# Performance work log

Measured on AMD Instinct MI355X. Metric: run time of the kernel, lower is better.

Reference implementation:

```python
import jax, jax.numpy as jnp
import numpy as np
import math

N_HEADS = 8

def setup_inputs() -> dict:
    key = jax.random.key(0)
    qkv = jax.random.normal(key, (4, 1536, 2048), dtype=jnp.float32)
    return {"qkv": qkv}

def reference(qkv):
    bs, width, length = qkv.shape
    ch = width // (3 * N_HEADS)
    # reshape to [bs*n_heads, 3*ch, length] then split into q, k, v
    qkv_h = qkv.reshape(bs * N_HEADS, 3 * ch, length)
    q = qkv_h[:, :ch]
    k = qkv_h[:, ch:2 * ch]
    v = qkv_h[:, 2 * ch:]
    scale = 1.0 / math.sqrt(math.sqrt(ch))
    # scores: [B*H, T, S]
    weight = jnp.einsum('bct,bcs->bts', q * scale, k * scale)
    weight = jax.nn.softmax(weight.astype(jnp.float32), axis=-1).astype(weight.dtype)
    a = jnp.einsum('bts,bcs->bct', weight, v)  # [B*H, ch, T]
    return a.reshape(bs, N_HEADS * ch, length)
```

## Files before the change

kernel.cpp:

```cpp
#include <hip/hip_runtime.h>
#include <hip/hip_bf16.h>

typedef __attribute__((ext_vector_type(8))) short bf16x8;
typedef __attribute__((ext_vector_type(8))) unsigned short u16x8;
typedef __attribute__((ext_vector_type(4))) float f32x4;
typedef __attribute__((ext_vector_type(16))) float f32x16;

#define SEQ 2048
#define NBH 32
#define QSCALE 0.1803368801111204f

#if __has_builtin(__builtin_amdgcn_exp2f)
#define EXP2(x) __builtin_amdgcn_exp2f(x)
#else
#define EXP2(x) exp2f(x)
#endif

__device__ __forceinline__ unsigned short bfc(float f) {
  union { __hip_bfloat16 h; unsigned short u; } v;
  v.h = __float2bfloat16(f);
  return v.u;
}

__global__ __launch_bounds__(256)
void prep_kernel(const float* __restrict__ qkv, unsigned short* __restrict__ ws) {
  const int tid = threadIdx.x;
  const int b = blockIdx.x;
  if (b < 4096) {
    int gid = b * 256 + tid;
    int sec = gid >> 19;
    int r = gid & 524287;
    int bh = r >> 14;
    int rr = r & 16383;
    int cc = rr >> 11;
    int t = rr & 2047;
    const float* src = qkv + ((size_t)(bh >> 3) * 1536 + (bh & 7) * 192 + sec * 64 + cc * 8) * SEQ + t;
    const float scale = sec ? 1.0f : QSCALE;
    u16x8 o;
    #pragma unroll
    for (int e = 0; e < 8; ++e) o[e] = bfc(src[(size_t)e * SEQ] * scale);
    if (sec == 0) {
      unsigned short* dst = ws + ((size_t)bh * SEQ + t) * 64;
      *(u16x8*)(dst + ((cc ^ (t & 7)) * 8)) = o;
    } else {
      const int tile = t >> 6, shh = (t >> 5) & 1, lww = t & 31;
      const int kc = cc >> 1, hh = cc & 1;
      unsigned short* dst = ws + (size_t)NBH * SEQ * 64 + (size_t)bh * SEQ * 64;
      const int idx = ((tile * 2 + shh) * 4 + kc) * 64 + hh * 32 + lww;
      *(u16x8*)(dst + (size_t)idx * 8) = o;
    }
  } else {
    int cid = (b - 4096) * 256 + tid;
    int bh = cid >> 14;
    int rr = cid & 16383;
    int c = rr >> 8;
    int cc = rr & 255;
    int tile = cc >> 3, sub = cc & 7;
    const float* src = qkv + ((size_t)(bh >> 3) * 1536 + (bh & 7) * 192 + 128 + c) * SEQ + cc * 8;
    float4 a = *(const float4*)(src);
    float4 bv = *(const float4*)(src + 4);
    u16x8 o;
    o[0] = bfc(a.x); o[1] = bfc(a.y); o[2] = bfc(a.z); o[3] = bfc(a.w);
    o[4] = bfc(bv.x); o[5] = bfc(bv.y); o[6] = bfc(bv.z); o[7] = bfc(bv.w);
    const int shh = sub >> 2, ks = (sub >> 1) & 1, hh = sub & 1;
    const int ch = c >> 5, lww = c & 31;
    unsigned short* dst = ws + (size_t)2 * NBH * SEQ * 64 + (size_t)bh * SEQ * 64;
    const int idx = (((tile * 2 + shh) * 2 + ch) * 2 + ks) * 64 + hh * 32 + lww;
    *(u16x8*)(dst + (size_t)idx * 8) = o;
  }
}

__global__ __launch_bounds__(256, 2)
void attn_main(const unsigned short* __restrict__ ws, float* __restrict__ out) {
  const int bid = blockIdx.x;
  const int bh = (bid & 7) + 8 * ((bid >> 3) >> 4);
  const int tile0 = (bid >> 3) & 15;
  const int t0 = tile0 * 128;

  const unsigned short* Qws = ws + ((size_t)bh * SEQ + t0) * 64;
  const unsigned short* Kf = ws + (size_t)NBH * SEQ * 64 + (size_t)bh * SEQ * 64;
  const unsigned short* Vf = ws + (size_t)2 * NBH * SEQ * 64 + (size_t)bh * SEQ * 64;
  float* __restrict__ outb = out + (size_t)bh * 64 * SEQ;

  __shared__ __align__(16) float red[8192];

  const int tid = threadIdx.x;
  const int w = tid >> 6;
  const int ts = w & 1;
  const int sh = w >> 1;
  const int l = tid & 63;
  const int lw = l & 31;
  const int h = l >> 5;
  const int sw = lw & 7;

  bf16x8 qB[2][4];
  #pragma unroll
  for (int tsub = 0; tsub < 2; ++tsub) {
    const int rloc = ts * 64 + tsub * 32 + lw;
    #pragma unroll
    for (int kc = 0; kc < 4; ++kc)
      qB[tsub][kc] = *(const bf16x8*)&Qws[rloc * 64 + (((2 * kc + h) ^ sw) * 8)];
  }

  f32x16 zero16;
  #pragma unroll
  for (int i = 0; i < 16; ++i) zero16[i] = 0.f;
  bf16x8 onesB;
  #pragma unroll
  for (int i = 0; i < 8; ++i) onesB[i] = (short)0x3F80;

  f32x16 accO[2][2];
  f32x16 psum[2];
  accO[0][0] = zero16; accO[0][1] = zero16;
  accO[1][0] = zero16; accO[1][1] = zero16;
  psum[0] = zero16; psum[1] = zero16;

  bf16x8 ka[4];
  #pragma unroll
  for (int kc = 0; kc < 4; ++kc)
    ka[kc] = *(const bf16x8*)&Kf[(size_t)((sh * 4 + kc) * 64 + l) * 8];

  #pragma unroll 1
  for (int it = 0; it < SEQ / 64; ++it) {
    bf16x8 kan[4];
    {
      const int itn = (it + 1) & 31;
      #pragma unroll
      for (int kc = 0; kc < 4; ++kc)
        kan[kc] = *(const bf16x8*)&Kf[(size_t)(((itn * 2 + sh) * 4 + kc) * 64 + l) * 8];
    }
    bf16x8 vB[2][2];
    #pragma unroll
    for (int ch = 0; ch < 2; ++ch)
      #pragma unroll
      for (int ks = 0; ks < 2; ++ks)
        vB[ch][ks] = *(const bf16x8*)&Vf[(size_t)(((((it * 2 + sh) * 2 + ch) * 2 + ks)) * 64 + l) * 8];

    f32x16 accS[2];
    #pragma unroll
    for (int kc = 0; kc < 4; ++kc) {
      #pragma unroll
      for (int tsub = 0; tsub < 2; ++tsub)
        accS[tsub] = __builtin_amdgcn_mfma_f32_32x32x16_bf16(
            ka[kc], qB[tsub][kc], kc ? accS[tsub] : zero16, 0, 0, 0);
    }

    #pragma unroll
    for (int tsub = 0; tsub < 2; ++tsub)
      #pragma unroll
      for (int r = 0; r < 16; ++r) accS[tsub][r] = EXP2(accS[tsub][r]);

    bf16x8 pA[2][2];
    #pragma unroll
    for (int tsub = 0; tsub < 2; ++tsub) {
      unsigned int pk[8];
      #pragma unroll
      for (int wd = 0; wd < 8; ++wd)
        asm("v_cvt_pk_bf16_f32 %0, %1, %2"
            : "=v"(pk[wd]) : "v"(accS[tsub][2 * wd]), "v"(accS[tsub][2 * wd + 1]));
      #pragma unroll
      for (int a = 0; a < 2; ++a) {
        unsigned int x0 = pk[4 * a + 0], y0 = pk[4 * a + 2];
        unsigned int x1 = pk[4 * a + 1], y1 = pk[4 * a + 3];
        asm("v_permlane32_swap_b32 %0, %1" : "+v"(x0), "+v"(y0));
        asm("v_permlane32_swap_b32 %0, %1" : "+v"(x1), "+v"(y1));
        union { unsigned int u[4]; bf16x8 v; } uu;
        uu.u[0] = x0; uu.u[1] = x1; uu.u[2] = y0; uu.u[3] = y1;
        pA[tsub][a] = uu.v;
      }
    }

    #pragma unroll
    for (int tsub = 0; tsub < 2; ++tsub)
      #pragma unroll
      for (int ks = 0; ks < 2; ++ks)
        psum[tsub] = __builtin_amdgcn_mfma_f32_32x32x16_bf16(pA[tsub][ks], onesB, psum[tsub], 0, 0, 0);

    #pragma unroll
    for (int ch = 0; ch < 2; ++ch) {
      #pragma unroll
      for (int ks = 0; ks < 2; ++ks) {
        #pragma unroll
        for (int tsub = 0; tsub < 2; ++tsub)
          accO[tsub][ch] = __builtin_amdgcn_mfma_f32_32x32x16_bf16(pA[tsub][ks], vB[ch][ks], accO[tsub][ch], 0, 0, 0);
      }
    }

    ka[0] = kan[0]; ka[1] = kan[1]; ka[2] = kan[2]; ka[3] = kan[3];
  }

  if (sh == 1) {
    #pragma unroll
    for (int tsub = 0; tsub < 2; ++tsub)
      #pragma unroll
      for (int ch = 0; ch < 2; ++ch)
        #pragma unroll
        for (int r = 0; r < 16; ++r)
          red[(((ts * 2 + tsub) * 2 + ch) * 16 + r) * 64 + l] = accO[tsub][ch][r];
  }
  __syncthreads();
  if (sh == 0) {
    #pragma unroll
    for (int tsub = 0; tsub < 2; ++tsub)
      #pragma unroll
      for (int ch = 0; ch < 2; ++ch)
        #pragma unroll
        for (int r = 0; r < 16; ++r)
          accO[tsub][ch][r] += red[(((ts * 2 + tsub) * 2 + ch) * 16 + r) * 64 + l];
  }
  __syncthreads();
  if (sh == 1) {
    #pragma unroll
    for (int tsub = 0; tsub < 2; ++tsub)
      #pragma unroll
      for (int r = 0; r < 16; ++r)
        red[((ts * 2 + tsub) * 16 + r) * 64 + l] = psum[tsub][r];
  }
  __syncthreads();
  if (sh == 0) {
    #pragma unroll
    for (int tsub = 0; tsub < 2; ++tsub) {
      float linv[16];
      #pragma unroll
      for (int r = 0; r < 16; ++r)
        linv[r] = 1.0f / (psum[tsub][r] + red[((ts * 2 + tsub) * 16 + r) * 64 + l]);
      #pragma unroll
      for (int ch = 0; ch < 2; ++ch) {
        #pragma unroll
        for (int r = 0; r < 16; ++r) {
          const int tg = t0 + ts * 64 + tsub * 32 + (r & 3) + 8 * (r >> 2) + 4 * h;
          outb[(size_t)(32 * ch + lw) * SEQ + tg] = accO[tsub][ch][r] * linv[r];
        }
      }
    }
  }
}

#define PAD 72
#define BTF 128
__device__ __forceinline__ unsigned short f2bf(float f) {
  union { float f; unsigned u; } v; v.f = f;
  return (unsigned short)((v.u + 0x7fffu + ((v.u >> 16) & 1u)) >> 16);
}

__global__ __launch_bounds__(512, 4)
void qkv_attn_fallback(const float* __restrict__ qkv, float* __restrict__ out) {
  const int bid = blockIdx.x;
  const int xcd = bid & 7;
  const int slot = bid >> 3;
  const int bh = xcd + 8 * (slot >> 4);
  const int tile = slot & 15;
  const int t0 = tile * BTF;

  const float* __restrict__ base = qkv + (size_t)((bh >> 3) * 1536 + (bh & 7) * 192) * SEQ;
  const float* __restrict__ qg = base;
  const float* __restrict__ kg = base + 64 * SEQ;
  const float* __restrict__ vg = base + 128 * SEQ;
  float* __restrict__ outb = out + (size_t)bh * 64 * SEQ;

  __shared__ __align__(16) unsigned short Qt[BTF * PAD];
  __shared__ __align__(16) unsigned short Kt[64 * PAD];
  __shared__ __align__(16) unsigned short Vt[64 * PAD];
  __shared__ __align__(16) unsigned short Pl[BTF * PAD];

  const int tid = threadIdx.x;
  const int w = tid >> 6;
  const int l = tid & 63;
  const int lr = l & 15;
  const int g = l >> 4;

  {
    const int cb = tid >> 5, tb = tid & 31;
    const int c0 = cb * 4, tt0 = tb * 4;
    const float* p = qg + c0 * SEQ + t0 + tt0;
    float4 r0 = *(const float4*)(p);
    float4 r1 = *(const float4*)(p + SEQ);
    float4 r2 = *(const float4*)(p + 2 * SEQ);
    float4 r3 = *(const float4*)(p + 3 * SEQ);
    const float s = 0.125f;
    ushort4 w0 = { f2bf(r0.x*s), f2bf(r1.x*s), f2bf(r2.x*s), f2bf(r3.x*s) };
    ushort4 w1 = { f2bf(r0.y*s), f2bf(r1.y*s), f2bf(r2.y*s), f2bf(r3.y*s) };
    ushort4 w2 = { f2bf(r0.z*s), f2bf(r1.z*s), f2bf(r2.z*s), f2bf(r3.z*s) };
    ushort4 w3 = { f2bf(r0.w*s), f2bf(r1.w*s), f2bf(r2.w*s), f2bf(r3.w*s) };
    *(ushort4*)&Qt[(tt0 + 0) * PAD + c0] = w0;
    *(ushort4*)&Qt[(tt0 + 1) * PAD + c0] = w1;
    *(ushort4*)&Qt[(tt0 + 2) * PAD + c0] = w2;
    *(ushort4*)&Qt[(tt0 + 3) * PAD + c0] = w3;
  }
  __syncthreads();

  bf16x8 qB0 = *(const bf16x8*)&Qt[(w * 16 + lr) * PAD + g * 8];
  bf16x8 qB1 = *(const bf16x8*)&Qt[(w * 16 + lr) * PAD + g * 8 + 32];

  f32x4 pv[4];
  #pragma unroll
  for (int i = 0; i < 4; ++i) pv[i] = (f32x4){0.f, 0.f, 0.f, 0.f};
  float mrun = -1e30f;
  float lsum = 0.f;

  for (int s0 = 0; s0 < SEQ; s0 += 64) {
    __syncthreads();
    {
      const int cb = tid >> 4, sb = tid & 15;
      const int c0 = cb * 2, sl = sb * 4;
      const float* p0 = kg + c0 * SEQ + s0 + sl;
      float4 a0 = *(const float4*)(p0);
      float4 a1 = *(const float4*)(p0 + SEQ);
      ushort2 y0 = { f2bf(a0.x), f2bf(a1.x) };
      ushort2 y1 = { f2bf(a0.y), f2bf(a1.y) };
      ushort2 y2 = { f2bf(a0.z), f2bf(a1.z) };
      ushort2 y3 = { f2bf(a0.w), f2bf(a1.w) };
      *(ushort2*)&Kt[(sl + 0) * PAD + c0] = y0;
      *(ushort2*)&Kt[(sl + 1) * PAD + c0] = y1;
      *(ushort2*)&Kt[(sl + 2) * PAD + c0] = y2;
      *(ushort2*)&Kt[(sl + 3) * PAD + c0] = y3;
    }
    {
      const int c = tid >> 3;
      const int sq = (tid & 7) * 8;
      const float* p0 = vg + c * SEQ + s0 + sq;
      float4 b0 = *(const float4*)(p0);
      float4 b1 = *(const float4*)(p0 + 4);
      ushort4 z0 = { f2bf(b0.x), f2bf(b0.y), f2bf(b0.z), f2bf(b0.w) };
      ushort4 z1 = { f2bf(b1.x), f2bf(b1.y), f2bf(b1.z), f2bf(b1.w) };
      *(ushort4*)&Vt[c * PAD + sq] = z0;
      *(ushort4*)&Vt[c * PAD + sq + 4] = z1;
    }
    __syncthreads();

    f32x4 acc[4];
    #pragma unroll
    for (int i = 0; i < 4; ++i) acc[i] = (f32x4){0.f, 0.f, 0.f, 0.f};
    #pragma unroll
    for (int ch = 0; ch < 2; ++ch) {
      bf16x8 qb = ch ? qB1 : qB0;
      #pragma unroll
      for (int sub = 0; sub < 4; ++sub) {
        bf16x8 ka = *(const bf16x8*)&Kt[(sub * 16 + lr) * PAD + g * 8 + 32 * ch];
        acc[sub] = __builtin_amdgcn_mfma_f32_16x16x32_bf16(ka, qb, acc[sub], 0, 0, 0);
      }
    }

    float pmax = -1e30f;
    #pragma unroll
    for (int sub = 0; sub < 4; ++sub)
      #pragma unroll
      for (int r = 0; r < 4; ++r) pmax = fmaxf(pmax, acc[sub][r]);
    pmax = fmaxf(pmax, __shfl_xor(pmax, 16));
    pmax = fmaxf(pmax, __shfl_xor(pmax, 32));
    const float mnew = fmaxf(mrun, pmax);
    const float alpha = __expf(mrun - mnew);
    float rsum = 0.f;
    #pragma unroll
    for (int sub = 0; sub < 4; ++sub) {
      #pragma unroll
      for (int r = 0; r < 4; ++r) {
        float p = __expf(acc[sub][r] - mnew);
        acc[sub][r] = p;
        rsum += p;
      }
    }
    rsum += __shfl_xor(rsum, 16);
    rsum += __shfl_xor(rsum, 32);
    lsum = lsum * alpha + rsum;
    mrun = mnew;

    #pragma unroll
    for (int sub = 0; sub < 4; ++sub) {
      ushort4 pw = { f2bf(acc[sub][0]), f2bf(acc[sub][1]), f2bf(acc[sub][2]), f2bf(acc[sub][3]) };
      *(ushort4*)&Pl[(w * 16 + lr) * PAD + sub * 16 + g * 4] = pw;
    }

    {
      const int sbase = (l & 48) + g * 4;
      #pragma unroll
      for (int r = 0; r < 4; ++r) {
        float ar = __shfl(alpha, sbase + r, 64);
        #pragma unroll
        for (int cs = 0; cs < 4; ++cs) pv[cs][r] *= ar;
      }
    }

    bf16x8 pA0 = *(const bf16x8*)&Pl[(w * 16 + lr) * PAD + g * 8];
    bf16x8 pA1 = *(const bf16x8*)&Pl[(w * 16 + lr) * PAD + g * 8 + 32];
    #pragma unroll
    for (int cs = 0; cs < 4; ++cs) {
      bf16x8 v0 = *(const bf16x8*)&Vt[(cs * 16 + lr) * PAD + g * 8];
      bf16x8 v1 = *(const bf16x8*)&Vt[(cs * 16 + lr) * PAD + g * 8 + 32];
      pv[cs] = __builtin_amdgcn_mfma_f32_16x16x32_bf16(pA0, v0, pv[cs], 0, 0, 0);
      pv[cs] = __builtin_amdgcn_mfma_f32_16x16x32_bf16(pA1, v1, pv[cs], 0, 0, 0);
    }
  }

  {
    const int sbase = (l & 48) + g * 4;
    float linv[4];
    #pragma unroll
    for (int r = 0; r < 4; ++r) linv[r] = 1.0f / __shfl(lsum, sbase + r, 64);
    #pragma unroll
    for (int cs = 0; cs < 4; ++cs) {
      #pragma unroll
      for (int r = 0; r < 4; ++r) {
        outb[(cs * 16 + lr) * SEQ + t0 + w * 16 + g * 4 + r] = pv[cs][r] * linv[r];
      }
    }
  }
}

extern "C" void kernel_launch(void* const* d_in, const int* in_sizes, int n_in,
                              void* d_out, int out_size, void* d_ws, size_t ws_size,
                              hipStream_t stream) {
  const float* qkv = (const float*)d_in[0];
  float* out = (float*)d_out;
  const size_t need = (size_t)3 * NBH * SEQ * 64 * sizeof(unsigned short);
  if (ws_size >= need) {
    unsigned short* ws = (unsigned short*)d_ws;
    prep_kernel<<<dim3(6144), dim3(256), 0, stream>>>(qkv, ws);
    attn_main<<<dim3(512), dim3(256), 0, stream>>>(ws, out);
  } else {
    qkv_attn_fallback<<<dim3(512), dim3(512), 0, stream>>>(qkv, out);
  }
}
```

Before: 65.01 us.

## Halve query tile per block to double grid and raise occupancy

The attention kernel's query tile per block drops from 128 to 64 rows, so each wave handles one 32-row subtile instead of two. The grid doubles to 1024 blocks, the shared reduction buffer halves, and launch bounds now allow 4 blocks per CU, aiming for more resident waves and better latency hiding. In exchange, each K/V tile is loaded twice as often per query row, which raises global/L2 traffic, and MFMA reuse of each K/V fragment is halved.

New measurement: 70.96 us. +9.2%, slower.

```diff
diff --git a/kernel.cpp b/kernel.cpp
--- a/kernel.cpp
+++ b/kernel.cpp
@@ -70,19 +70,19 @@
   }
 }
 
-__global__ __launch_bounds__(256, 2)
+__global__ __launch_bounds__(256, 4)
 void attn_main(const unsigned short* __restrict__ ws, float* __restrict__ out) {
   const int bid = blockIdx.x;
-  const int bh = (bid & 7) + 8 * ((bid >> 3) >> 4);
-  const int tile0 = (bid >> 3) & 15;
-  const int t0 = tile0 * 128;
+  const int bh = (bid & 7) + 8 * ((bid >> 3) >> 5);
+  const int tile0 = (bid >> 3) & 31;
+  const int t0 = tile0 * 64;
 
   const unsigned short* Qws = ws + ((size_t)bh * SEQ + t0) * 64;
   const unsigned short* Kf = ws + (size_t)NBH * SEQ * 64 + (size_t)bh * SEQ * 64;
   const unsigned short* Vf = ws + (size_t)2 * NBH * SEQ * 64 + (size_t)bh * SEQ * 64;
   float* __restrict__ outb = out + (size_t)bh * 64 * SEQ;
 
-  __shared__ __align__(16) float red[8192];
+  __shared__ __align__(16) float red[4096];
 
   const int tid = threadIdx.x;
   const int w = tid >> 6;
@@ -93,13 +93,12 @@
   const int h = l >> 5;
   const int sw = lw & 7;
 
-  bf16x8 qB[2][4];
-  #pragma unroll
-  for (int tsub = 0; tsub < 2; ++tsub) {
-    const int rloc = ts * 64 + tsub * 32 + lw;
+  bf16x8 qB[4];
+  {
+    const int rloc = ts * 32 + lw;
     #pragma unroll
     for (int kc = 0; kc < 4; ++kc)
-      qB[tsub][kc] = *(const bf16x8*)&Qws[rloc * 64 + (((2 * kc + h) ^ sw) * 8)];
+      qB[kc] = *(const bf16x8*)&Qws[rloc * 64 + (((2 * kc + h) ^ sw) * 8)];
   }
 
   f32x16 zero16;
@@ -109,11 +108,9 @@
   #pragma unroll
   for (int i = 0; i < 8; ++i) onesB[i] = (short)0x3F80;
 
-  f32x16 accO[2][2];
-  f32x16 psum[2];
-  accO[0][0] = zero16; accO[0][1] = zero16;
-  accO[1][0] = zero16; accO[1][1] = zero16;
-  psum[0] = zero16; psum[1] = zero16;
+  f32x16 accO[2];
+  f32x16 psum;
+  accO[0] = zero16; accO[1] = zero16; psum = zero16;
 
   bf16x8 ka[4];
   #pragma unroll
@@ -136,28 +133,21 @@
       for (int ks = 0; ks < 2; ++ks)
         vB[ch][ks] = *(const bf16x8*)&Vf[(size_t)(((((it * 2 + sh) * 2 + ch) * 2 + ks)) * 64 + l) * 8];
 
-    f32x16 accS[2];
-    #pragma unroll
-    for (int kc = 0; kc < 4; ++kc) {
-      #pragma unroll
-      for (int tsub = 0; tsub < 2; ++tsub)
-        accS[tsub] = __builtin_amdgcn_mfma_f32_32x32x16_bf16(
-            ka[kc], qB[tsub][kc], kc ? accS[tsub] : zero16, 0, 0, 0);
-    }
-
-    #pragma unroll
-    for (int tsub = 0; tsub < 2; ++tsub)
-      #pragma unroll
-      for (int r = 0; r < 16; ++r) accS[tsub][r] = EXP2(accS[tsub][r]);
-
-    bf16x8 pA[2][2];
-    #pragma unroll
-    for (int tsub = 0; tsub < 2; ++tsub) {
+    f32x16 accS;
+    #pragma unroll
+    for (int kc = 0; kc < 4; ++kc)
+      accS = __builtin_amdgcn_mfma_f32_32x32x16_bf16(ka[kc], qB[kc], kc ? accS : zero16, 0, 0, 0);
+
+    #pragma unroll
+    for (int r = 0; r < 16; ++r) accS[r] = EXP2(accS[r]);
+
+    bf16x8 pA[2];
+    {
       unsigned int pk[8];
       #pragma unroll
       for (int wd = 0; wd < 8; ++wd)
         asm("v_cvt_pk_bf16_f32 %0, %1, %2"
-            : "=v"(pk[wd]) : "v"(accS[tsub][2 * wd]), "v"(accS[tsub][2 * wd + 1]));
+            : "=v"(pk[wd]) : "v"(accS[2 * wd]), "v"(accS[2 * wd + 1]));
       #pragma unroll
       for (int a = 0; a < 2; ++a) {
         unsigned int x0 = pk[4 * a + 0], y0 = pk[4 * a + 2];
@@ -166,71 +156,56 @@
         asm("v_permlane32_swap_b32 %0, %1" : "+v"(x1), "+v"(y1));
         union { unsigned int u[4]; bf16x8 v; } uu;
         uu.u[0] = x0; uu.u[1] = x1; uu.u[2] = y0; uu.u[3] = y1;
-        pA[tsub][a] = uu.v;
-      }
-    }
-
-    #pragma unroll
-    for (int tsub = 0; tsub < 2; ++tsub)
+        pA[a] = uu.v;
+      }
+    }
+
+    #pragma unroll
+    for (int ks = 0; ks < 2; ++ks)
+      psum = __builtin_amdgcn_mfma_f32_32x32x16_bf16(pA[ks], onesB, psum, 0, 0, 0);
+
+    #pragma unroll
+    for (int ch = 0; ch < 2; ++ch)
       #pragma unroll
       for (int ks = 0; ks < 2; ++ks)
-        psum[tsub] = __builtin_amdgcn_mfma_f32_32x32x16_bf16(pA[tsub][ks], onesB, psum[tsub], 0, 0, 0);
-
-    #pragma unroll
-    for (int ch = 0; ch < 2; ++ch) {
-      #pragma unroll
-      for (int ks = 0; ks < 2; ++ks) {
-        #pragma unroll
-        for (int tsub = 0; tsub < 2; ++tsub)
-          accO[tsub][ch] = __builtin_amdgcn_mfma_f32_32x32x16_bf16(pA[tsub][ks], vB[ch][ks], accO[tsub][ch], 0, 0, 0);
-      }
-    }
+        accO[ch] = __builtin_amdgcn_mfma_f32_32x32x16_bf16(pA[ks], vB[ch][ks], accO[ch], 0, 0, 0);
 
     ka[0] = kan[0]; ka[1] = kan[1]; ka[2] = kan[2]; ka[3] = kan[3];
   }
 
   if (sh == 1) {
     #pragma unroll
-    for (int tsub = 0; tsub < 2; ++tsub)
-      #pragma unroll
-      for (int ch = 0; ch < 2; ++ch)
-        #pragma unroll
-        for (int r = 0; r < 16; ++r)
-          red[(((ts * 2 + tsub) * 2 + ch) * 16 + r) * 64 + l] = accO[tsub][ch][r];
+    for (int ch = 0; ch < 2; ++ch)
+      #pragma unroll
+      for (int r = 0; r < 16; ++r)
+        red[((ts * 2 + ch) * 16 + r) * 64 + l] = accO[ch][r];
   }
   __syncthreads();
   if (sh == 0) {
     #pragma unroll
-    for (int tsub = 0; tsub < 2; ++tsub)
-      #pragma unroll
-      for (int ch = 0; ch < 2; ++ch)
-        #pragma unroll
-        for (int r = 0; r < 16; ++r)
-          accO[tsub][ch][r] += red[(((ts * 2 + tsub) * 2 + ch) * 16 + r) * 64 + l];
+    for (int ch = 0; ch < 2; ++ch)
+      #pragma unroll
+      for (int r = 0; r < 16; ++r)
+        accO[ch][r] += red[((ts * 2 + ch) * 16 + r) * 64 + l];
   }
   __syncthreads();
   if (sh == 1) {
     #pragma unroll
-    for (int tsub = 0; tsub < 2; ++tsub)
-      #pragma unroll
-      for (int r = 0; r < 16; ++r)
-        red[((ts * 2 + tsub) * 16 + r) * 64 + l] = psum[tsub][r];
+    for (int r = 0; r < 16; ++r)
+      red[(ts * 16 + r) * 64 + l] = psum[r];
   }
   __syncthreads();
   if (sh == 0) {
-    #pragma unroll
-    for (int tsub = 0; tsub < 2; ++tsub) {
-      float linv[16];
-      #pragma unroll
-      for (int r = 0; r < 16; ++r)
-        linv[r] = 1.0f / (psum[tsub][r] + red[((ts * 2 + tsub) * 16 + r) * 64 + l]);
-      #pragma unroll
-      for (int ch = 0; ch < 2; ++ch) {
-        #pragma unroll
-        for (int r = 0; r < 16; ++r) {
-          const int tg = t0 + ts * 64 + tsub * 32 + (r & 3) + 8 * (r >> 2) + 4 * h;
-          outb[(size_t)(32 * ch + lw) * SEQ + tg] = accO[tsub][ch][r] * linv[r];
-        }
+    float linv[16];
+    #pragma unroll
+    for (int r = 0; r < 16; ++r)
+      linv[r] = 1.0f / (psum[r] + red[(ts * 16 + r) * 64 + l]);
+    #pragma unroll
+    for (int ch = 0; ch < 2; ++ch) {
+      #pragma unroll
+      for (int r = 0; r < 16; ++r) {
+        const int tg = t0 + ts * 32 + (r & 3) + 8 * (r >> 2) + 4 * h;
+        outb[(size_t)(32 * ch + lw) * SEQ + tg] = accO[ch][r] * linv[r];
       }
     }
   }
@@ -416,7 +391,7 @@
   if (ws_size >= need) {
     unsigned short* ws = (unsigned short*)d_ws;
     prep_kernel<<<dim3(6144), dim3(256), 0, stream>>>(qkv, ws);
-    attn_main<<<dim3(512), dim3(256), 0, stream>>>(ws, out);
+    attn_main<<<dim3(1024), dim3(256), 0, stream>>>(ws, out);
   } else {
     qkv_attn_fallback<<<dim3(512), dim3(512), 0, stream>>>(qkv, out);
   }
```
